# Kernel tuning notes

Measured on AMD Instinct MI355X. Metric: run time of the kernel, lower is better.

## Reference

```python
import jax, jax.numpy as jnp
import numpy as np

B, C, H, W = 16, 512, 14, 14
OUT = 8192
EPS_SQRT = 1e-5
EPS_NORM = 1e-12


def _make_sketch(key, input_dim, output_dim):
    kh, ks = jax.random.split(key)
    rand_h = jax.random.randint(kh, (input_dim,), 0, output_dim)
    rand_s = (2 * jax.random.randint(ks, (input_dim,), 0, 2) - 1).astype(jnp.float32)
    # count-sketch matrix densified: one nonzero (+-1) per row
    S = jnp.zeros((input_dim, output_dim), dtype=jnp.float32)
    return S.at[jnp.arange(input_dim), rand_h].set(rand_s)


def setup_inputs() -> dict:
    key = jax.random.key(0)
    kx, k1, k2 = jax.random.split(key, 3)
    x = jax.random.normal(kx, (B, C, H, W), dtype=jnp.float32)
    sketch1 = _make_sketch(k1, C, OUT)
    sketch2 = _make_sketch(k2, C, OUT)
    return {"x": x, "sketch1": sketch1, "sketch2": sketch2}


def reference(x, sketch1, sketch2):
    output_dim = sketch1.shape[1]
    # [B,C,H,W] -> [B,H,W,C] then project with count-sketch matrices -> [B,H,W,OUT]
    xp = jnp.transpose(x, (0, 2, 3, 1))
    p1 = xp @ sketch1
    p2 = xp @ sketch2
    # circular convolution via FFT (torch.rfft unnormalized; torch.irfft has 1/n, then *output_dim)
    f1 = jnp.fft.rfft(p1, axis=-1)
    f2 = jnp.fft.rfft(p2, axis=-1)
    cbp = jnp.fft.irfft(f1 * f2, n=output_dim, axis=-1) * output_dim
    # sum-pool over spatial dims -> [B, OUT]
    X = cbp.sum(axis=(1, 2))
    # signed square-root
    X = jnp.sign(X) * jnp.sqrt(jnp.abs(X) + EPS_SQRT)
    # L2 normalize per row (F.normalize semantics)
    norm = jnp.maximum(jnp.linalg.norm(X, axis=-1, keepdims=True), EPS_NORM)
    return X / norm
```

## Files before the change

kernel.cpp:

```cpp
#include <hip/hip_runtime.h>
#include <math.h>

#define OUT_DIM 8192
#define C_DIM   512
#define B_DIM   16
#define HW      196
#define KPAD    224
#define LROW    40

typedef __attribute__((ext_vector_type(8))) short bf16x8;
typedef __attribute__((ext_vector_type(4))) float f32x4;

__global__ __launch_bounds__(256) void prep(
    const float* __restrict__ x,
    const float* __restrict__ S1, const float* __restrict__ S2,
    int* __restrict__ h1, float* __restrict__ s1,
    int* __restrict__ h2, float* __restrict__ s2,
    unsigned short* __restrict__ xhi, unsigned short* __restrict__ xlo,
    float* __restrict__ accum, float* __restrict__ ss)
{
    const int bid = blockIdx.x;
    const int t = threadIdx.x;

    if (bid < 1024) {
        int row = bid & 511;
        const float* S = (bid < 512) ? S1 : S2;
        int* h = (bid < 512) ? h1 : h2;
        float* s = (bid < 512) ? s1 : s2;
        const float4* p = (const float4*)(S + (size_t)row * OUT_DIM);
#pragma unroll
        for (int m = 0; m < 8; ++m) {
            int q = t + m * 256;
            float4 v = p[q];
            int base = q * 4;
            if (v.x != 0.f) { h[row] = base + 0; s[row] = v.x; }
            if (v.y != 0.f) { h[row] = base + 1; s[row] = v.y; }
            if (v.z != 0.f) { h[row] = base + 2; s[row] = v.z; }
            if (v.w != 0.f) { h[row] = base + 3; s[row] = v.w; }
        }
    } else if (bid < 1280) {
        int u = bid - 1024;
        int rowg = u * 32 + (t >> 3);
        int kq = t & 7;
        int k0 = kq * 28;
        unsigned short hb[28], lb[28];
        if (kq < 7) {
            const float* src = x + (size_t)rowg * HW + k0;
#pragma unroll
            for (int q = 0; q < 7; ++q) {
                float4 v = *(const float4*)(src + q * 4);
                float vv[4] = {v.x, v.y, v.z, v.w};
#pragma unroll
                for (int e = 0; e < 4; ++e) {
                    unsigned int ub = __float_as_uint(vv[e]);
                    unsigned short hi = (unsigned short)(ub >> 16);
                    float hif = __uint_as_float(((unsigned int)hi) << 16);
                    float lof = vv[e] - hif;
                    unsigned short lo = (unsigned short)(__float_as_uint(lof) >> 16);
                    hb[q * 4 + e] = hi;
                    lb[q * 4 + e] = lo;
                }
            }
        } else {
#pragma unroll
            for (int e = 0; e < 28; ++e) { hb[e] = 0; lb[e] = 0; }
        }
        unsigned short* dh = xhi + (size_t)rowg * KPAD + k0;
        unsigned short* dl = xlo + (size_t)rowg * KPAD + k0;
#pragma unroll
        for (int q = 0; q < 7; ++q) {
            *(ushort4*)(dh + q * 4) = make_ushort4(hb[q*4], hb[q*4+1], hb[q*4+2], hb[q*4+3]);
            *(ushort4*)(dl + q * 4) = make_ushort4(lb[q*4], lb[q*4+1], lb[q*4+2], lb[q*4+3]);
        }
    } else {
        int z = bid - 1280;
#pragma unroll
        for (int i = 0; i < 16; ++i)
            accum[z * 4096 + t + i * 256] = 0.f;
        if (z == 0 && t < 16) ss[t] = 0.f;
    }
}

__global__ __launch_bounds__(256) void gram_mfma(
    const unsigned short* __restrict__ xhi, const unsigned short* __restrict__ xlo,
    const int* __restrict__ h1, const float* __restrict__ s1,
    const int* __restrict__ h2, const float* __restrict__ s2,
    float* __restrict__ accum)
{
    __shared__ __align__(16) unsigned short lds[4 * 128 * LROW];

    const int bid = blockIdx.x;
    const int xcd = bid & 7;
    const int idx = bid >> 3;
    const int b   = xcd + 8 * (idx & 1);
    const int tile = idx >> 1;
    const int i1 = tile >> 2, i2 = tile & 3;
    const int c1b = i1 * 128, c2b = i2 * 128;

    const int t = threadIdx.x;
    const int l = t & 63, w = t >> 6;
    const int wr = w >> 1, wc = w & 1;
    const int lrow = l & 15, lk = l >> 4;

    const size_t xbase = (size_t)b * C_DIM * KPAD;

    f32x4 acc[4][4];
#pragma unroll
    for (int m = 0; m < 4; ++m)
#pragma unroll
        for (int n = 0; n < 4; ++n) acc[m][n] = (f32x4){0.f, 0.f, 0.f, 0.f};

    for (int kc = 0; kc < 7; ++kc) {
        __syncthreads();
#pragma unroll
        for (int m = 0; m < 8; ++m) {
            int u = t + m * 256;
            int ts  = u >> 9;
            int rem = u & 511;
            int row = rem >> 2;
            int grp = rem & 3;
            int cb = (ts < 2) ? c1b : c2b;
            const unsigned short* sp = (ts & 1) ? xlo : xhi;
            bf16x8 v = *(const bf16x8*)(sp + xbase + (size_t)(cb + row) * KPAD + kc * 32 + grp * 8);
            *(bf16x8*)(lds + ts * (128 * LROW) + row * LROW + grp * 8) = v;
        }
        __syncthreads();

        bf16x8 ah[4], al[4], bh[4], bl[4];
#pragma unroll
        for (int m = 0; m < 4; ++m) {
            int r = wr * 64 + m * 16 + lrow;
            ah[m] = *(const bf16x8*)(lds + 0 * (128 * LROW) + r * LROW + lk * 8);
            al[m] = *(const bf16x8*)(lds + 1 * (128 * LROW) + r * LROW + lk * 8);
        }
#pragma unroll
        for (int n = 0; n < 4; ++n) {
            int r = wc * 64 + n * 16 + lrow;
            bh[n] = *(const bf16x8*)(lds + 2 * (128 * LROW) + r * LROW + lk * 8);
            bl[n] = *(const bf16x8*)(lds + 3 * (128 * LROW) + r * LROW + lk * 8);
        }
#pragma unroll
        for (int m = 0; m < 4; ++m)
#pragma unroll
            for (int n = 0; n < 4; ++n) {
                acc[m][n] = __builtin_amdgcn_mfma_f32_16x16x32_bf16(ah[m], bh[n], acc[m][n], 0, 0, 0);
                acc[m][n] = __builtin_amdgcn_mfma_f32_16x16x32_bf16(ah[m], bl[n], acc[m][n], 0, 0, 0);
                acc[m][n] = __builtin_amdgcn_mfma_f32_16x16x32_bf16(al[m], bh[n], acc[m][n], 0, 0, 0);
            }
    }

    int   hh1[4][4]; float sv1[4][4];
    int   hh2[4];    float sv2[4];
#pragma unroll
    for (int m = 0; m < 4; ++m)
#pragma unroll
        for (int r = 0; r < 4; ++r) {
            int c1 = c1b + wr * 64 + m * 16 + lk * 4 + r;
            hh1[m][r] = h1[c1]; sv1[m][r] = s1[c1];
        }
#pragma unroll
    for (int n = 0; n < 4; ++n) {
        int c2 = c2b + wc * 64 + n * 16 + lrow;
        hh2[n] = h2[c2]; sv2[n] = s2[c2];
    }

    __syncthreads();
    float* bins = (float*)lds;
    for (int mm = t; mm < OUT_DIM; mm += 256) bins[mm] = 0.f;
    __syncthreads();
#pragma unroll
    for (int m = 0; m < 4; ++m)
#pragma unroll
        for (int n = 0; n < 4; ++n)
#pragma unroll
            for (int r = 0; r < 4; ++r) {
                int bin = (hh1[m][r] + hh2[n]) & (OUT_DIM - 1);
                atomicAdd(&bins[bin], acc[m][n][r] * sv1[m][r] * sv2[n]);
            }
    __syncthreads();

    float* ab = accum + (size_t)b * OUT_DIM;
    for (int mm = t; mm < OUT_DIM; mm += 256) atomicAdd(&ab[mm], bins[mm]);
}

__global__ __launch_bounds__(256) void fin_a(
    const float* __restrict__ accum, float* __restrict__ ss)
{
    const int b = blockIdx.x >> 4, ch = blockIdx.x & 15, t = threadIdx.x;
    float p = 0.f;
#pragma unroll
    for (int i = 0; i < 2; ++i) {
        int k = ch * 512 + t + i * 256;
        float a = accum[(size_t)b * OUT_DIM + k] * (float)OUT_DIM;
        p += fabsf(a) + 1e-5f;
    }
#pragma unroll
    for (int off = 32; off; off >>= 1) p += __shfl_down(p, off, 64);
    __shared__ float red[4];
    if ((t & 63) == 0) red[t >> 6] = p;
    __syncthreads();
    if (t == 0) atomicAdd(&ss[b], red[0] + red[1] + red[2] + red[3]);
}

__global__ __launch_bounds__(256) void fin_b(
    const float* __restrict__ accum, const float* __restrict__ ss,
    float* __restrict__ out)
{
    const int b = blockIdx.x >> 4, ch = blockIdx.x & 15, t = threadIdx.x;
    float inv = 1.f / fmaxf(sqrtf(ss[b]), 1e-12f);
#pragma unroll
    for (int i = 0; i < 2; ++i) {
        int k = ch * 512 + t + i * 256;
        float a = accum[(size_t)b * OUT_DIM + k] * (float)OUT_DIM;
        float sg = (a > 0.f) ? 1.f : ((a < 0.f) ? -1.f : 0.f);
        out[(size_t)b * OUT_DIM + k] = sg * sqrtf(fabsf(a) + 1e-5f) * inv;
    }
}

extern "C" void kernel_launch(void* const* d_in, const int* in_sizes, int n_in,
                              void* d_out, int out_size, void* d_ws, size_t ws_size,
                              hipStream_t stream) {
    const float* x   = (const float*)d_in[0];
    const float* sk1 = (const float*)d_in[1];
    const float* sk2 = (const float*)d_in[2];

    char* ws = (char*)d_ws;
    int*   h1 = (int*)(ws);
    float* s1 = (float*)(ws + 2048);
    int*   h2 = (int*)(ws + 4096);
    float* s2 = (float*)(ws + 6144);
    float* ss = (float*)(ws + 8192);
    float* accum = (float*)(ws + 8448);
    unsigned short* xhi = (unsigned short*)(ws + 532736);
    unsigned short* xlo = (unsigned short*)(ws + 4202752);

    prep<<<1312, 256, 0, stream>>>(x, sk1, sk2, h1, s1, h2, s2, xhi, xlo, accum, ss);
    gram_mfma<<<256, 256, 0, stream>>>(xhi, xlo, h1, s1, h2, s2, accum);
    fin_a<<<256, 256, 0, stream>>>(accum, ss);
    fin_b<<<256, 256, 0, stream>>>(accum, ss, (float*)d_out);
}
```

Baseline: 130.3 us.

## Fuse bf16 split into gram kernel, use per-tile partials instead of atomics

The gram kernel now loads fp32 x directly, splits each value into hi/lo bf16 in registers, and prefetches the next K-chunk during the MFMA phase. This removes the separate xhi/xlo conversion pass and its workspace traffic. The block grows to 512 threads with 8 waves, each owning a 64x32 subtile. Global atomics into accum are replaced by plain per-tile partial writes, which fin_a reduces while also computing the signed sqrt, so fin_b only scales; the cost is 16x more partial buffer reads in fin_a.

```diff
diff --git a/kernel.cpp b/kernel.cpp
--- a/kernel.cpp
+++ b/kernel.cpp
@@ -5,144 +5,129 @@
 #define C_DIM   512
 #define B_DIM   16
 #define HW      196
-#define KPAD    224
 #define LROW    40
+#define PL      (128 * LROW)
 
 typedef __attribute__((ext_vector_type(8))) short bf16x8;
 typedef __attribute__((ext_vector_type(4))) float f32x4;
 
 __global__ __launch_bounds__(256) void prep(
-    const float* __restrict__ x,
     const float* __restrict__ S1, const float* __restrict__ S2,
     int* __restrict__ h1, float* __restrict__ s1,
     int* __restrict__ h2, float* __restrict__ s2,
-    unsigned short* __restrict__ xhi, unsigned short* __restrict__ xlo,
-    float* __restrict__ accum, float* __restrict__ ss)
+    float* __restrict__ ss)
 {
     const int bid = blockIdx.x;
     const int t = threadIdx.x;
-
-    if (bid < 1024) {
-        int row = bid & 511;
-        const float* S = (bid < 512) ? S1 : S2;
-        int* h = (bid < 512) ? h1 : h2;
-        float* s = (bid < 512) ? s1 : s2;
-        const float4* p = (const float4*)(S + (size_t)row * OUT_DIM);
-#pragma unroll
-        for (int m = 0; m < 8; ++m) {
-            int q = t + m * 256;
-            float4 v = p[q];
-            int base = q * 4;
-            if (v.x != 0.f) { h[row] = base + 0; s[row] = v.x; }
-            if (v.y != 0.f) { h[row] = base + 1; s[row] = v.y; }
-            if (v.z != 0.f) { h[row] = base + 2; s[row] = v.z; }
-            if (v.w != 0.f) { h[row] = base + 3; s[row] = v.w; }
-        }
-    } else if (bid < 1280) {
-        int u = bid - 1024;
-        int rowg = u * 32 + (t >> 3);
-        int kq = t & 7;
-        int k0 = kq * 28;
-        unsigned short hb[28], lb[28];
-        if (kq < 7) {
-            const float* src = x + (size_t)rowg * HW + k0;
-#pragma unroll
-            for (int q = 0; q < 7; ++q) {
-                float4 v = *(const float4*)(src + q * 4);
-                float vv[4] = {v.x, v.y, v.z, v.w};
-#pragma unroll
-                for (int e = 0; e < 4; ++e) {
-                    unsigned int ub = __float_as_uint(vv[e]);
-                    unsigned short hi = (unsigned short)(ub >> 16);
-                    float hif = __uint_as_float(((unsigned int)hi) << 16);
-                    float lof = vv[e] - hif;
-                    unsigned short lo = (unsigned short)(__float_as_uint(lof) >> 16);
-                    hb[q * 4 + e] = hi;
-                    lb[q * 4 + e] = lo;
-                }
-            }
-        } else {
-#pragma unroll
-            for (int e = 0; e < 28; ++e) { hb[e] = 0; lb[e] = 0; }
-        }
-        unsigned short* dh = xhi + (size_t)rowg * KPAD + k0;
-        unsigned short* dl = xlo + (size_t)rowg * KPAD + k0;
-#pragma unroll
-        for (int q = 0; q < 7; ++q) {
-            *(ushort4*)(dh + q * 4) = make_ushort4(hb[q*4], hb[q*4+1], hb[q*4+2], hb[q*4+3]);
-            *(ushort4*)(dl + q * 4) = make_ushort4(lb[q*4], lb[q*4+1], lb[q*4+2], lb[q*4+3]);
-        }
-    } else {
-        int z = bid - 1280;
-#pragma unroll
-        for (int i = 0; i < 16; ++i)
-            accum[z * 4096 + t + i * 256] = 0.f;
-        if (z == 0 && t < 16) ss[t] = 0.f;
-    }
-}
-
-__global__ __launch_bounds__(256) void gram_mfma(
-    const unsigned short* __restrict__ xhi, const unsigned short* __restrict__ xlo,
+    int row = bid & 511;
+    const float* S = (bid < 512) ? S1 : S2;
+    int* h = (bid < 512) ? h1 : h2;
+    float* s = (bid < 512) ? s1 : s2;
+    const float4* p = (const float4*)(S + (size_t)row * OUT_DIM);
+#pragma unroll
+    for (int m = 0; m < 8; ++m) {
+        int q = t + m * 256;
+        float4 v = p[q];
+        int base = q * 4;
+        if (v.x != 0.f) { h[row] = base + 0; s[row] = v.x; }
+        if (v.y != 0.f) { h[row] = base + 1; s[row] = v.y; }
+        if (v.z != 0.f) { h[row] = base + 2; s[row] = v.z; }
+        if (v.w != 0.f) { h[row] = base + 3; s[row] = v.w; }
+    }
+    if (bid == 0 && t < B_DIM) ss[t] = 0.f;
+}
+
+__global__ __launch_bounds__(512) void gram_mfma(
+    const float* __restrict__ x,
     const int* __restrict__ h1, const float* __restrict__ s1,
     const int* __restrict__ h2, const float* __restrict__ s2,
-    float* __restrict__ accum)
-{
-    __shared__ __align__(16) unsigned short lds[4 * 128 * LROW];
+    float* __restrict__ partials)
+{
+    __shared__ __align__(16) unsigned short lds[4 * PL];
 
     const int bid = blockIdx.x;
     const int xcd = bid & 7;
     const int idx = bid >> 3;
     const int b   = xcd + 8 * (idx & 1);
     const int tile = idx >> 1;
-    const int i1 = tile >> 2, i2 = tile & 3;
-    const int c1b = i1 * 128, c2b = i2 * 128;
+    const int c1b = (tile >> 2) * 128, c2b = (tile & 3) * 128;
 
     const int t = threadIdx.x;
     const int l = t & 63, w = t >> 6;
-    const int wr = w >> 1, wc = w & 1;
+    const int wr = w >> 2, wc = w & 3;
     const int lrow = l & 15, lk = l >> 4;
 
-    const size_t xbase = (size_t)b * C_DIM * KPAD;
-
-    f32x4 acc[4][4];
+    const float* xb = x + (size_t)b * C_DIM * HW;
+
+    const int row0 = t >> 2, grp0 = t & 3;
+    const float* srcA = xb + (size_t)(c1b + row0) * HW + grp0 * 8;
+    const float* srcB = xb + (size_t)(c2b + row0) * HW + grp0 * 8;
+
+    f32x4 acc[4][2];
 #pragma unroll
     for (int m = 0; m < 4; ++m)
 #pragma unroll
-        for (int n = 0; n < 4; ++n) acc[m][n] = (f32x4){0.f, 0.f, 0.f, 0.f};
-
+        for (int n = 0; n < 2; ++n) acc[m][n] = (f32x4){0.f, 0.f, 0.f, 0.f};
+
+    float4 a0, a1, b0, b1;
+    const float4 z4 = make_float4(0.f, 0.f, 0.f, 0.f);
+
+    a0 = *(const float4*)(srcA);     a1 = *(const float4*)(srcA + 4);
+    b0 = *(const float4*)(srcB);     b1 = *(const float4*)(srcB + 4);
+
+#pragma unroll
     for (int kc = 0; kc < 7; ++kc) {
         __syncthreads();
-#pragma unroll
-        for (int m = 0; m < 8; ++m) {
-            int u = t + m * 256;
-            int ts  = u >> 9;
-            int rem = u & 511;
-            int row = rem >> 2;
-            int grp = rem & 3;
-            int cb = (ts < 2) ? c1b : c2b;
-            const unsigned short* sp = (ts & 1) ? xlo : xhi;
-            bf16x8 v = *(const bf16x8*)(sp + xbase + (size_t)(cb + row) * KPAD + kc * 32 + grp * 8);
-            *(bf16x8*)(lds + ts * (128 * LROW) + row * LROW + grp * 8) = v;
+        {
+            float va[8] = {a0.x, a0.y, a0.z, a0.w, a1.x, a1.y, a1.z, a1.w};
+            float vb[8] = {b0.x, b0.y, b0.z, b0.w, b1.x, b1.y, b1.z, b1.w};
+            bf16x8 ahv, alv, bhv, blv;
+#pragma unroll
+            for (int e = 0; e < 8; ++e) {
+                unsigned int ua = __float_as_uint(va[e]);
+                float haf = __uint_as_float(ua & 0xFFFF0000u);
+                ahv[e] = (short)(ua >> 16);
+                alv[e] = (short)(__float_as_uint(va[e] - haf) >> 16);
+                unsigned int ub = __float_as_uint(vb[e]);
+                float hbf = __uint_as_float(ub & 0xFFFF0000u);
+                bhv[e] = (short)(ub >> 16);
+                blv[e] = (short)(__float_as_uint(vb[e] - hbf) >> 16);
+            }
+            unsigned short* dst = lds + row0 * LROW + grp0 * 8;
+            *(bf16x8*)(dst + 0 * PL) = ahv;
+            *(bf16x8*)(dst + 1 * PL) = alv;
+            *(bf16x8*)(dst + 2 * PL) = bhv;
+            *(bf16x8*)(dst + 3 * PL) = blv;
         }
         __syncthreads();
-
-        bf16x8 ah[4], al[4], bh[4], bl[4];
+        if (kc < 6) {
+            const int kn = (kc + 1) * 32;
+            if (kc + 1 < 6) {
+                a0 = *(const float4*)(srcA + kn); a1 = *(const float4*)(srcA + kn + 4);
+                b0 = *(const float4*)(srcB + kn); b1 = *(const float4*)(srcB + kn + 4);
+            } else {
+                a1 = z4; b1 = z4;
+                a0 = (grp0 == 0) ? *(const float4*)(srcA + 192) : z4;
+                b0 = (grp0 == 0) ? *(const float4*)(srcB + 192) : z4;
+            }
+        }
+        bf16x8 ah[4], al[4], bh[2], bl[2];
 #pragma unroll
         for (int m = 0; m < 4; ++m) {
             int r = wr * 64 + m * 16 + lrow;
-            ah[m] = *(const bf16x8*)(lds + 0 * (128 * LROW) + r * LROW + lk * 8);
-            al[m] = *(const bf16x8*)(lds + 1 * (128 * LROW) + r * LROW + lk * 8);
-        }
-#pragma unroll
-        for (int n = 0; n < 4; ++n) {
-            int r = wc * 64 + n * 16 + lrow;
-            bh[n] = *(const bf16x8*)(lds + 2 * (128 * LROW) + r * LROW + lk * 8);
-            bl[n] = *(const bf16x8*)(lds + 3 * (128 * LROW) + r * LROW + lk * 8);
+            ah[m] = *(const bf16x8*)(lds + 0 * PL + r * LROW + lk * 8);
+            al[m] = *(const bf16x8*)(lds + 1 * PL + r * LROW + lk * 8);
+        }
+#pragma unroll
+        for (int n = 0; n < 2; ++n) {
+            int r = wc * 32 + n * 16 + lrow;
+            bh[n] = *(const bf16x8*)(lds + 2 * PL + r * LROW + lk * 8);
+            bl[n] = *(const bf16x8*)(lds + 3 * PL + r * LROW + lk * 8);
         }
 #pragma unroll
         for (int m = 0; m < 4; ++m)
 #pragma unroll
-            for (int n = 0; n < 4; ++n) {
+            for (int n = 0; n < 2; ++n) {
                 acc[m][n] = __builtin_amdgcn_mfma_f32_16x16x32_bf16(ah[m], bh[n], acc[m][n], 0, 0, 0);
                 acc[m][n] = __builtin_amdgcn_mfma_f32_16x16x32_bf16(ah[m], bl[n], acc[m][n], 0, 0, 0);
                 acc[m][n] = __builtin_amdgcn_mfma_f32_16x16x32_bf16(al[m], bh[n], acc[m][n], 0, 0, 0);
@@ -150,7 +135,7 @@
     }
 
     int   hh1[4][4]; float sv1[4][4];
-    int   hh2[4];    float sv2[4];
+    int   hh2[2];    float sv2[2];
 #pragma unroll
     for (int m = 0; m < 4; ++m)
 #pragma unroll
@@ -159,19 +144,19 @@
             hh1[m][r] = h1[c1]; sv1[m][r] = s1[c1];
         }
 #pragma unroll
-    for (int n = 0; n < 4; ++n) {
-        int c2 = c2b + wc * 64 + n * 16 + lrow;
+    for (int n = 0; n < 2; ++n) {
+        int c2 = c2b + wc * 32 + n * 16 + lrow;
         hh2[n] = h2[c2]; sv2[n] = s2[c2];
     }
 
     __syncthreads();
     float* bins = (float*)lds;
-    for (int mm = t; mm < OUT_DIM; mm += 256) bins[mm] = 0.f;
+    for (int mm = t; mm < OUT_DIM; mm += 512) bins[mm] = 0.f;
     __syncthreads();
 #pragma unroll
     for (int m = 0; m < 4; ++m)
 #pragma unroll
-        for (int n = 0; n < 4; ++n)
+        for (int n = 0; n < 2; ++n)
 #pragma unroll
             for (int r = 0; r < 4; ++r) {
                 int bin = (hh1[m][r] + hh2[n]) & (OUT_DIM - 1);
@@ -179,41 +164,51 @@
             }
     __syncthreads();
 
-    float* ab = accum + (size_t)b * OUT_DIM;
-    for (int mm = t; mm < OUT_DIM; mm += 256) atomicAdd(&ab[mm], bins[mm]);
+    float* outp = partials + (size_t)(b * 16 + tile) * OUT_DIM;
+    for (int mm = t; mm < OUT_DIM; mm += 512) outp[mm] = bins[mm];
 }
 
 __global__ __launch_bounds__(256) void fin_a(
-    const float* __restrict__ accum, float* __restrict__ ss)
+    float* __restrict__ partials, float* __restrict__ ss)
 {
     const int b = blockIdx.x >> 4, ch = blockIdx.x & 15, t = threadIdx.x;
-    float p = 0.f;
+    float sq = 0.f;
+    float vals[2];
+    int ks[2];
 #pragma unroll
     for (int i = 0; i < 2; ++i) {
-        int k = ch * 512 + t + i * 256;
-        float a = accum[(size_t)b * OUT_DIM + k] * (float)OUT_DIM;
-        p += fabsf(a) + 1e-5f;
-    }
-#pragma unroll
-    for (int off = 32; off; off >>= 1) p += __shfl_down(p, off, 64);
+        int k = ch * 512 + i * 256 + t;
+        ks[i] = k;
+        float a = 0.f;
+#pragma unroll
+        for (int tile = 0; tile < 16; ++tile)
+            a += partials[(size_t)(b * 16 + tile) * OUT_DIM + k];
+        a *= (float)OUT_DIM;
+        float sg = (a > 0.f) ? 1.f : ((a < 0.f) ? -1.f : 0.f);
+        vals[i] = sg * sqrtf(fabsf(a) + 1e-5f);
+        sq += fabsf(a) + 1e-5f;
+    }
+#pragma unroll
+    for (int off = 32; off; off >>= 1) sq += __shfl_down(sq, off, 64);
     __shared__ float red[4];
-    if ((t & 63) == 0) red[t >> 6] = p;
+    if ((t & 63) == 0) red[t >> 6] = sq;
     __syncthreads();
     if (t == 0) atomicAdd(&ss[b], red[0] + red[1] + red[2] + red[3]);
+#pragma unroll
+    for (int i = 0; i < 2; ++i)
+        partials[(size_t)(b * 16) * OUT_DIM + ks[i]] = vals[i];
 }
 
 __global__ __launch_bounds__(256) void fin_b(
-    const float* __restrict__ accum, const float* __restrict__ ss,
+    const float* __restrict__ partials, const float* __restrict__ ss,
     float* __restrict__ out)
 {
     const int b = blockIdx.x >> 4, ch = blockIdx.x & 15, t = threadIdx.x;
     float inv = 1.f / fmaxf(sqrtf(ss[b]), 1e-12f);
 #pragma unroll
     for (int i = 0; i < 2; ++i) {
-        int k = ch * 512 + t + i * 256;
-        float a = accum[(size_t)b * OUT_DIM + k] * (float)OUT_DIM;
-        float sg = (a > 0.f) ? 1.f : ((a < 0.f) ? -1.f : 0.f);
-        out[(size_t)b * OUT_DIM + k] = sg * sqrtf(fabsf(a) + 1e-5f) * inv;
+        int k = ch * 512 + i * 256 + t;
+        out[(size_t)b * OUT_DIM + k] = partials[(size_t)(b * 16) * OUT_DIM + k] * inv;
     }
 }
 
@@ -230,12 +225,10 @@
     int*   h2 = (int*)(ws + 4096);
     float* s2 = (float*)(ws + 6144);
     float* ss = (float*)(ws + 8192);
-    float* accum = (float*)(ws + 8448);
-    unsigned short* xhi = (unsigned short*)(ws + 532736);
-    unsigned short* xlo = (unsigned short*)(ws + 4202752);
-
-    prep<<<1312, 256, 0, stream>>>(x, sk1, sk2, h1, s1, h2, s2, xhi, xlo, accum, ss);
-    gram_mfma<<<256, 256, 0, stream>>>(xhi, xlo, h1, s1, h2, s2, accum);
-    fin_a<<<256, 256, 0, stream>>>(accum, ss);
-    fin_b<<<256, 256, 0, stream>>>(accum, ss, (float*)d_out);
-}
+    float* partials = (float*)(ws + 8448);
+
+    prep<<<1024, 256, 0, stream>>>(sk1, sk2, h1, s1, h2, s2, ss);
+    gram_mfma<<<256, 512, 0, stream>>>(x, h1, s1, h2, s2, partials);
+    fin_a<<<256, 256, 0, stream>>>(partials, ss);
+    fin_b<<<256, 256, 0, stream>>>(partials, ss, (float*)d_out);
+}
```

New measurement: 121.3 us. 1.07x faster.
